# Kernel optimization log

Measured on AMD Instinct MI355X. Metric: run time of the kernel, lower is better.

The kernel has to match this reference:

```python
import jax, jax.numpy as jnp
import numpy as np

B, N, C_IN, C_OUT = 8, 4096, 512, 512


def setup_inputs() -> dict:
    key = jax.random.key(0)
    k1, k2, k3, k4 = jax.random.split(key, 4)
    node_features = jax.random.normal(k1, (B, N, C_IN), dtype=jnp.float32)
    # positive edge weights -> strictly positive degrees
    adj_matrix = jax.random.uniform(k2, (B, N, N), dtype=jnp.float32)
    W = jax.random.normal(k3, (C_IN, C_OUT), dtype=jnp.float32) / np.sqrt(C_IN)
    b = jax.random.normal(k4, (C_OUT,), dtype=jnp.float32) * 0.01
    return {"node_features": node_features, "adj_matrix": adj_matrix, "W": W, "b": b}


def reference(node_features, adj_matrix, W, b):
    # degree (row-sum of adjacency), kept as [B, N, 1] for broadcasting
    num_neighbours = adj_matrix.sum(axis=-1, keepdims=True)
    # linear projection: [B, N, c_in] @ [c_in, c_out] + b
    h = jnp.einsum("bni,io->bno", node_features, W) + b
    # adjacency aggregation: [B, N, N] @ [B, N, c_out]
    h = jnp.einsum("bnm,bmo->bno", adj_matrix, h)
    # mean over neighbours
    return h / num_neighbours
```

## Files before the change

### kernel.cpp

```cpp
#include <hip/hip_runtime.h>
#include <stdint.h>


typedef __attribute__((ext_vector_type(4))) float  f32x4;
typedef __attribute__((ext_vector_type(8))) __bf16 bf16x8;
typedef __attribute__((ext_vector_type(4))) __bf16 bf16x4;

#define GLOAD_LDS16(gsrc, ldst)                                                           \
  __builtin_amdgcn_global_load_lds((const __attribute__((address_space(1))) void*)(gsrc), \
                                   (__attribute__((address_space(3))) void*)(ldst), 16, 0, 0)

#define BARRIER                                  \
  do {                                           \
    asm volatile("" ::: "memory");               \
    __builtin_amdgcn_s_barrier();                \
    asm volatile("" ::: "memory");               \
  } while (0)

__global__ void __launch_bounds__(256) k_wt(const float* __restrict__ W,
                                            __bf16* __restrict__ Wt) {
  __shared__ __bf16 t[64][65];
  const int k0 = blockIdx.x * 64, n0 = blockIdx.y * 64;
  const int tid = threadIdx.x;
  const int r = tid >> 2, c4 = (tid & 3) * 16;
#pragma unroll
  for (int j = 0; j < 4; ++j) {
    f32x4 v = *reinterpret_cast<const f32x4*>(W + (size_t)(k0 + r) * 512 + n0 + c4 + j * 4);
#pragma unroll
    for (int q = 0; q < 4; ++q) t[c4 + j * 4 + q][r] = (__bf16)v[q];
  }
  __syncthreads();
#pragma unroll
  for (int j = 0; j < 4; ++j) {
    bf16x4 o;
#pragma unroll
    for (int q = 0; q < 4; ++q) o[q] = t[r][c4 + j * 4 + q];
    *reinterpret_cast<bf16x4*>(Wt + (size_t)(n0 + r) * 512 + k0 + c4 + j * 4) = o;
  }
}

__global__ void __launch_bounds__(256) k_proj(const float* __restrict__ X,
                                              const __bf16* __restrict__ Wt,
                                              const float* __restrict__ bias,
                                              __bf16* __restrict__ hT) {
  __shared__ __attribute__((aligned(16))) __bf16 Xs[128][72];
  __shared__ __attribute__((aligned(16))) __bf16 Ws[128][72];
  const int n0 = blockIdx.x * 128;
  const int m0 = blockIdx.y * 128;
  const int tid = threadIdx.x;
  const int lane = tid & 63, w = tid >> 6;
  const int wr = w >> 1, wc = w & 1;
  const int srow = tid >> 1, scb = (tid & 1) * 32;

  f32x4 acc[4][4] = {};

  for (int k0 = 0; k0 < 512; k0 += 64) {
    const float* xp = X + (size_t)(m0 + srow) * 512 + k0 + scb;
    f32x4 xv[8];
#pragma unroll
    for (int j = 0; j < 8; ++j) xv[j] = *reinterpret_cast<const f32x4*>(xp + j * 4);
#pragma unroll
    for (int q = 0; q < 4; ++q) {
      bf16x8 o;
#pragma unroll
      for (int e = 0; e < 8; ++e) { const int idx = q * 8 + e; o[e] = (__bf16)xv[idx >> 2][idx & 3]; }
      *reinterpret_cast<bf16x8*>(&Xs[srow][scb + q * 8]) = o;
    }
    const __bf16* wp = Wt + (size_t)(n0 + srow) * 512 + k0 + scb;
#pragma unroll
    for (int q = 0; q < 4; ++q)
      *reinterpret_cast<bf16x8*>(&Ws[srow][scb + q * 8]) =
          *reinterpret_cast<const bf16x8*>(wp + q * 8);
    __syncthreads();

    for (int kk = 0; kk < 64; kk += 32) {
      const int ko = kk + ((lane >> 4) << 3);
      bf16x8 a[4], bb[4];
#pragma unroll
      for (int i = 0; i < 4; ++i)
        a[i] = *reinterpret_cast<const bf16x8*>(&Xs[wr * 64 + i * 16 + (lane & 15)][ko]);
#pragma unroll
      for (int j = 0; j < 4; ++j)
        bb[j] = *reinterpret_cast<const bf16x8*>(&Ws[wc * 64 + j * 16 + (lane & 15)][ko]);
#pragma unroll
      for (int i = 0; i < 4; ++i)
#pragma unroll
        for (int j = 0; j < 4; ++j)
          acc[i][j] = __builtin_amdgcn_mfma_f32_16x16x32_bf16(a[i], bb[j], acc[i][j], 0, 0, 0);
    }
    __syncthreads();
  }

  float bj[4];
#pragma unroll
  for (int j = 0; j < 4; ++j) bj[j] = bias[n0 + wc * 64 + j * 16 + (lane & 15)];
  const int batch = m0 >> 12;
  const int mloc0 = (m0 & 4095) + wr * 64;
#pragma unroll
  for (int i = 0; i < 4; ++i) {
    const int m_in = mloc0 + i * 16 + ((lane >> 4) << 2);
#pragma unroll
    for (int j = 0; j < 4; ++j) {
      const int n = n0 + wc * 64 + j * 16 + (lane & 15);
      bf16x4 o;
#pragma unroll
      for (int r = 0; r < 4; ++r) o[r] = (__bf16)(acc[i][j][r] + bj[j]);
      *reinterpret_cast<bf16x4*>(hT + ((size_t)batch * 512 + n) * 4096 + m_in) = o;
    }
  }
}

__global__ void __launch_bounds__(1024, 4) k_agg(const float* __restrict__ adj,
                                                 const __bf16* __restrict__ hT,
                                                 float* __restrict__ out) {
  __shared__ __attribute__((aligned(16))) char lds[163840];
  char* As0 = lds;
  char* As1 = lds + 16384;
  char* Hs0 = lds + 32768;
  char* Hs1 = lds + 98304;

  const int bx = ((int)blockIdx.x & 7) * 32 + ((int)blockIdx.x >> 3);
  const int batch = bx >> 5;
  const int m0 = (bx & 31) * 128;
  const int tid = threadIdx.x;
  const int lane = tid & 63, w = tid >> 6;
  const int wr = w >> 3, wc = w & 7;

  const float*  adjb = adj + (size_t)batch * 4096 * 4096;
  const __bf16* hTb  = hT + (size_t)batch * 512 * 4096;
  float* outb = out + (size_t)batch * 4096 * 512;

  const int arow = tid >> 3;
  const int acb  = (tid & 7) * 8;
  const int aw   = arow * 128 + (((acb * 2)) ^ ((arow & 7) << 4));
  const float* adjrow = adjb + (size_t)(m0 + arow) * 4096 + acb;

  const int srcblk = (((lane & 7) ^ ((lane >> 3) & 7)) << 3);
  const int hrow_l = (lane >> 3);

  const int koffbase = (lane >> 4) << 3;
  const int kswz = (lane & 7) << 4;

  f32x4 acc[4][4] = {};
  float pdeg = 0.f;
  f32x4 av[2];

  auto load_adj = [&](int k0) {
    av[0] = __builtin_nontemporal_load(reinterpret_cast<const f32x4*>(adjrow + k0));
    av[1] = __builtin_nontemporal_load(reinterpret_cast<const f32x4*>(adjrow + k0 + 4));
  };
  auto issue_hs = [&](int k0, char* Hn) {
#pragma unroll
    for (int q = 0; q < 4; ++q) {
      const int c = w * 4 + q;
      const __bf16* src = hTb + (size_t)(c * 8 + hrow_l) * 4096 + k0 + srcblk;
      GLOAD_LDS16(src, Hn + c * 1024);
    }
  };
  auto write_as = [&](char* An) {
    bf16x8 o0;
#pragma unroll
    for (int e = 0; e < 8; ++e) o0[e] = (__bf16)av[e >> 2][e & 3];
    float s = 0.f;
#pragma unroll
    for (int e = 0; e < 8; ++e) s += av[e >> 2][e & 3];
    pdeg += s;
    *reinterpret_cast<bf16x8*>(An + aw) = o0;
  };
  auto compute = [&](const char* Ac, const char* Hc) {
#pragma unroll
    for (int kk = 0; kk < 64; kk += 32) {
      const int ko2 = ((kk + koffbase) * 2) ^ kswz;
      bf16x8 a[4], bb[4];
#pragma unroll
      for (int i = 0; i < 4; ++i) {
        const int row = wr * 64 + i * 16 + (lane & 15);
        a[i] = *reinterpret_cast<const bf16x8*>(Ac + row * 128 + ko2);
      }
#pragma unroll
      for (int j = 0; j < 4; ++j) {
        const int orow = wc * 64 + j * 16 + (lane & 15);
        bb[j] = *reinterpret_cast<const bf16x8*>(Hc + orow * 128 + ko2);
      }
#pragma unroll
      for (int i = 0; i < 4; ++i)
#pragma unroll
        for (int j = 0; j < 4; ++j)
          acc[i][j] = __builtin_amdgcn_mfma_f32_16x16x32_bf16(a[i], bb[j], acc[i][j], 0, 0, 0);
    }
  };

  load_adj(0);
  issue_hs(0, Hs0);
  write_as(As0);
  asm volatile("s_waitcnt vmcnt(0)" ::: "memory");
  asm volatile("s_waitcnt lgkmcnt(0)" ::: "memory");
  BARRIER;

  for (int t = 0; t < 63; ++t) {
    const int cur = t & 1;
    const char* Ac = cur ? As1 : As0;
    const char* Hc = cur ? Hs1 : Hs0;
    char* An = cur ? As0 : As1;
    char* Hn = cur ? Hs0 : Hs1;

    load_adj((t + 1) * 64);
    issue_hs((t + 1) * 64, Hn);
    compute(Ac, Hc);
    write_as(An);
    asm volatile("s_waitcnt vmcnt(0)" ::: "memory");
    asm volatile("s_waitcnt lgkmcnt(0)" ::: "memory");
    BARRIER;
  }

  compute(As1, Hs1);

  float d = pdeg;
  d += __shfl_xor(d, 1, 64);
  d += __shfl_xor(d, 2, 64);
  d += __shfl_xor(d, 4, 64);
  __syncthreads();
  if ((tid & 7) == 0) reinterpret_cast<float*>(lds)[arow] = d;
  __syncthreads();
  const float* degf = reinterpret_cast<const float*>(lds);

#pragma unroll
  for (int i = 0; i < 4; ++i) {
    const int rbase = wr * 64 + i * 16 + ((lane >> 4) << 2);
    float rd[4];
#pragma unroll
    for (int r = 0; r < 4; ++r) rd[r] = 1.0f / degf[rbase + r];
#pragma unroll
    for (int j = 0; j < 4; ++j) {
      const int o = wc * 64 + j * 16 + (lane & 15);
#pragma unroll
      for (int r = 0; r < 4; ++r)
        __builtin_nontemporal_store(acc[i][j][r] * rd[r],
                                    &outb[(size_t)(m0 + rbase + r) * 512 + o]);
    }
  }
}

extern "C" void kernel_launch(void* const* d_in, const int* in_sizes, int n_in,
                              void* d_out, int out_size, void* d_ws, size_t ws_size,
                              hipStream_t stream) {
  (void)in_sizes; (void)n_in; (void)out_size; (void)ws_size;
  const float* X    = (const float*)d_in[0];
  const float* adj  = (const float*)d_in[1];
  const float* W    = (const float*)d_in[2];
  const float* bias = (const float*)d_in[3];
  float* out = (float*)d_out;

  char* ws = (char*)d_ws;
  __bf16* hT = (__bf16*)ws;
  __bf16* Wt = (__bf16*)(ws + (size_t)32 * 1024 * 1024);

  k_wt<<<dim3(8, 8), 256, 0, stream>>>(W, Wt);
  k_proj<<<dim3(4, 256), 256, 0, stream>>>(X, Wt, bias, hT);
  k_agg<<<dim3(256), 1024, 0, stream>>>(adj, hT, out);
}
```

Measured before the change: 235.7 us.

## Prefetch adjacency tiles two iterations ahead with partial vmcnt waits

Adjacency loads now go into two alternating register sets and are issued two tiles ahead instead of one. The loop is unrolled by two to switch register sets, and it waits only on vmcnt(2), so the newest adjacency loads stay in flight across the barrier. This is meant to hide the global-memory latency of the large fp32 adjacency stream behind more MFMA work. It costs extra VGPRs and depends on the order in which memory counters complete, including the LDS-direct loads.

New measurement: 271.5 us. 15.2% more time.

```diff
diff --git a/kernel.cpp b/kernel.cpp
--- a/kernel.cpp
+++ b/kernel.cpp
@@ -143,12 +143,8 @@
 
   f32x4 acc[4][4] = {};
   float pdeg = 0.f;
-  f32x4 av[2];
-
-  auto load_adj = [&](int k0) {
-    av[0] = __builtin_nontemporal_load(reinterpret_cast<const f32x4*>(adjrow + k0));
-    av[1] = __builtin_nontemporal_load(reinterpret_cast<const f32x4*>(adjrow + k0 + 4));
-  };
+  f32x4 avA0, avA1, avB0, avB1;
+
   auto issue_hs = [&](int k0, char* Hn) {
 #pragma unroll
     for (int q = 0; q < 4; ++q) {
@@ -157,16 +153,6 @@
       GLOAD_LDS16(src, Hn + c * 1024);
     }
   };
-  auto write_as = [&](char* An) {
-    bf16x8 o0;
-#pragma unroll
-    for (int e = 0; e < 8; ++e) o0[e] = (__bf16)av[e >> 2][e & 3];
-    float s = 0.f;
-#pragma unroll
-    for (int e = 0; e < 8; ++e) s += av[e >> 2][e & 3];
-    pdeg += s;
-    *reinterpret_cast<bf16x8*>(An + aw) = o0;
-  };
   auto compute = [&](const char* Ac, const char* Hc) {
 #pragma unroll
     for (int kk = 0; kk < 64; kk += 32) {
@@ -190,30 +176,65 @@
     }
   };
 
-  load_adj(0);
+#define TILE_BODY(T, AVU0, AVU1, AVL0, AVL1, DOLOAD)                                      \
+  do {                                                                                    \
+    const int cur_ = (T) & 1;                                                             \
+    const char* Ac_ = cur_ ? As1 : As0;                                                   \
+    const char* Hc_ = cur_ ? Hs1 : Hs0;                                                   \
+    char* An_ = cur_ ? As0 : As1;                                                         \
+    char* Hn_ = cur_ ? Hs0 : Hs1;                                                         \
+    issue_hs(((T) + 1) * 64, Hn_);                                                        \
+    __builtin_amdgcn_sched_barrier(0);                \
+    if (DOLOAD) {                                                                         \
+      AVL0 = __builtin_nontemporal_load(                                                  \
+          reinterpret_cast<const f32x4*>(adjrow + ((T) + 2) * 64));                       \
+      AVL1 = __builtin_nontemporal_load(                                                  \
+          reinterpret_cast<const f32x4*>(adjrow + ((T) + 2) * 64 + 4));                   \
+    }                                                                                     \
+    compute(Ac_, Hc_);                                                                    \
+    {                                                                                     \
+      bf16x8 o0_;                                                                         \
+      _Pragma("unroll") for (int e = 0; e < 4; ++e) o0_[e] = (__bf16)AVU0[e];             \
+      _Pragma("unroll") for (int e = 0; e < 4; ++e) o0_[4 + e] = (__bf16)AVU1[e];         \
+      pdeg += AVU0[0] + AVU0[1] + AVU0[2] + AVU0[3] +                                     \
+              AVU1[0] + AVU1[1] + AVU1[2] + AVU1[3];                                      \
+      *reinterpret_cast<bf16x8*>(An_ + aw) = o0_;                                         \
+    }                                                                                     \
+    if (DOLOAD) { asm volatile("s_waitcnt vmcnt(2)" ::: "memory"); }                      \
+    else        { asm volatile("s_waitcnt vmcnt(0)" ::: "memory"); }                      \
+    asm volatile("s_waitcnt lgkmcnt(0)" ::: "memory");                                    \
+    BARRIER;                                                                              \
+  } while (0)
+
   issue_hs(0, Hs0);
-  write_as(As0);
-  asm volatile("s_waitcnt vmcnt(0)" ::: "memory");
+  __builtin_amdgcn_sched_barrier(0);
+  avA0 = __builtin_nontemporal_load(reinterpret_cast<const f32x4*>(adjrow));
+  avA1 = __builtin_nontemporal_load(reinterpret_cast<const f32x4*>(adjrow + 4));
+  {
+    bf16x8 o0;
+#pragma unroll
+    for (int e = 0; e < 4; ++e) o0[e] = (__bf16)avA0[e];
+#pragma unroll
+    for (int e = 0; e < 4; ++e) o0[4 + e] = (__bf16)avA1[e];
+    pdeg += avA0[0] + avA0[1] + avA0[2] + avA0[3] +
+            avA1[0] + avA1[1] + avA1[2] + avA1[3];
+    *reinterpret_cast<bf16x8*>(As0 + aw) = o0;
+  }
+  avA0 = __builtin_nontemporal_load(reinterpret_cast<const f32x4*>(adjrow + 64));
+  avA1 = __builtin_nontemporal_load(reinterpret_cast<const f32x4*>(adjrow + 68));
+  asm volatile("s_waitcnt vmcnt(2)" ::: "memory");
   asm volatile("s_waitcnt lgkmcnt(0)" ::: "memory");
   BARRIER;
 
-  for (int t = 0; t < 63; ++t) {
-    const int cur = t & 1;
-    const char* Ac = cur ? As1 : As0;
-    const char* Hc = cur ? Hs1 : Hs0;
-    char* An = cur ? As0 : As1;
-    char* Hn = cur ? Hs0 : Hs1;
-
-    load_adj((t + 1) * 64);
-    issue_hs((t + 1) * 64, Hn);
-    compute(Ac, Hc);
-    write_as(An);
-    asm volatile("s_waitcnt vmcnt(0)" ::: "memory");
-    asm volatile("s_waitcnt lgkmcnt(0)" ::: "memory");
-    BARRIER;
-  }
-
+  for (int tp = 0; tp < 31; ++tp) {
+    const int t0 = 2 * tp;
+    TILE_BODY(t0,     avA0, avA1, avB0, avB1, true);
+    TILE_BODY(t0 + 1, avB0, avB1, avA0, avA1, true);
+  }
+  TILE_BODY(62, avA0, avA1, avB0, avB1, false);
   compute(As1, Hs1);
+
+#undef TILE_BODY
 
   float d = pdeg;
   d += __shfl_xor(d, 1, 64);
```

## Load H operand directly from global into registers instead of staging in LDS

Applied to the files above, without the earlier changes.

The aggregation kernel no longer stages the transposed projection tile in double-buffered LDS via global_load_lds. Each wave now reads its B-fragments straight from global memory (expected to hit L2), which shrinks LDS from 160KB to about 33KB and removes the H-tile copy and its explicit waitcnt/barrier sequence. In exchange, every wave issues redundant global reads for the same H data with less latency hiding, since those loads sit directly in the MFMA loop.

Measured after the change: 394.8 us. 1.68x slower.

```diff
diff --git a/kernel.cpp b/kernel.cpp
--- a/kernel.cpp
+++ b/kernel.cpp
@@ -5,17 +5,6 @@
 typedef __attribute__((ext_vector_type(4))) float  f32x4;
 typedef __attribute__((ext_vector_type(8))) __bf16 bf16x8;
 typedef __attribute__((ext_vector_type(4))) __bf16 bf16x4;
-
-#define GLOAD_LDS16(gsrc, ldst)                                                           \
-  __builtin_amdgcn_global_load_lds((const __attribute__((address_space(1))) void*)(gsrc), \
-                                   (__attribute__((address_space(3))) void*)(ldst), 16, 0, 0)
-
-#define BARRIER                                  \
-  do {                                           \
-    asm volatile("" ::: "memory");               \
-    __builtin_amdgcn_s_barrier();                \
-    asm volatile("" ::: "memory");               \
-  } while (0)
 
 __global__ void __launch_bounds__(256) k_wt(const float* __restrict__ W,
                                             __bf16* __restrict__ Wt) {
@@ -113,11 +102,9 @@
 __global__ void __launch_bounds__(1024, 4) k_agg(const float* __restrict__ adj,
                                                  const __bf16* __restrict__ hT,
                                                  float* __restrict__ out) {
-  __shared__ __attribute__((aligned(16))) char lds[163840];
+  __shared__ __attribute__((aligned(16))) char lds[33280];
   char* As0 = lds;
   char* As1 = lds + 16384;
-  char* Hs0 = lds + 32768;
-  char* Hs1 = lds + 98304;
 
   const int bx = ((int)blockIdx.x & 7) * 32 + ((int)blockIdx.x >> 3);
   const int batch = bx >> 5;
@@ -132,42 +119,32 @@
 
   const int arow = tid >> 3;
   const int acb  = (tid & 7) * 8;
-  const int aw   = arow * 128 + (((acb * 2)) ^ ((arow & 7) << 4));
+  const int aw   = arow * 128 + ((acb * 2) ^ ((arow & 7) << 4));
   const float* adjrow = adjb + (size_t)(m0 + arow) * 4096 + acb;
-
-  const int srcblk = (((lane & 7) ^ ((lane >> 3) & 7)) << 3);
-  const int hrow_l = (lane >> 3);
 
   const int koffbase = (lane >> 4) << 3;
   const int kswz = (lane & 7) << 4;
 
+  const __bf16* hTw = hTb + (size_t)(wc * 64 + (lane & 15)) * 4096 + ((lane >> 4) << 3);
+
   f32x4 acc[4][4] = {};
   float pdeg = 0.f;
-  f32x4 av[2];
+  f32x4 av0, av1;
 
   auto load_adj = [&](int k0) {
-    av[0] = __builtin_nontemporal_load(reinterpret_cast<const f32x4*>(adjrow + k0));
-    av[1] = __builtin_nontemporal_load(reinterpret_cast<const f32x4*>(adjrow + k0 + 4));
-  };
-  auto issue_hs = [&](int k0, char* Hn) {
-#pragma unroll
-    for (int q = 0; q < 4; ++q) {
-      const int c = w * 4 + q;
-      const __bf16* src = hTb + (size_t)(c * 8 + hrow_l) * 4096 + k0 + srcblk;
-      GLOAD_LDS16(src, Hn + c * 1024);
-    }
+    av0 = __builtin_nontemporal_load(reinterpret_cast<const f32x4*>(adjrow + k0));
+    av1 = __builtin_nontemporal_load(reinterpret_cast<const f32x4*>(adjrow + k0 + 4));
   };
   auto write_as = [&](char* An) {
     bf16x8 o0;
 #pragma unroll
-    for (int e = 0; e < 8; ++e) o0[e] = (__bf16)av[e >> 2][e & 3];
-    float s = 0.f;
-#pragma unroll
-    for (int e = 0; e < 8; ++e) s += av[e >> 2][e & 3];
-    pdeg += s;
+    for (int e = 0; e < 4; ++e) o0[e] = (__bf16)av0[e];
+#pragma unroll
+    for (int e = 0; e < 4; ++e) o0[4 + e] = (__bf16)av1[e];
+    pdeg += av0[0] + av0[1] + av0[2] + av0[3] + av1[0] + av1[1] + av1[2] + av1[3];
     *reinterpret_cast<bf16x8*>(An + aw) = o0;
   };
-  auto compute = [&](const char* Ac, const char* Hc) {
+  auto compute = [&](const char* Ac, int kbase) {
 #pragma unroll
     for (int kk = 0; kk < 64; kk += 32) {
       const int ko2 = ((kk + koffbase) * 2) ^ kswz;
@@ -178,10 +155,8 @@
         a[i] = *reinterpret_cast<const bf16x8*>(Ac + row * 128 + ko2);
       }
 #pragma unroll
-      for (int j = 0; j < 4; ++j) {
-        const int orow = wc * 64 + j * 16 + (lane & 15);
-        bb[j] = *reinterpret_cast<const bf16x8*>(Hc + orow * 128 + ko2);
-      }
+      for (int j = 0; j < 4; ++j)
+        bb[j] = *reinterpret_cast<const bf16x8*>(hTw + (size_t)j * 16 * 4096 + kbase + kk);
 #pragma unroll
       for (int i = 0; i < 4; ++i)
 #pragma unroll
@@ -191,29 +166,20 @@
   };
 
   load_adj(0);
-  issue_hs(0, Hs0);
   write_as(As0);
-  asm volatile("s_waitcnt vmcnt(0)" ::: "memory");
-  asm volatile("s_waitcnt lgkmcnt(0)" ::: "memory");
-  BARRIER;
+  __syncthreads();
 
   for (int t = 0; t < 63; ++t) {
     const int cur = t & 1;
     const char* Ac = cur ? As1 : As0;
-    const char* Hc = cur ? Hs1 : Hs0;
     char* An = cur ? As0 : As1;
-    char* Hn = cur ? Hs0 : Hs1;
 
     load_adj((t + 1) * 64);
-    issue_hs((t + 1) * 64, Hn);
-    compute(Ac, Hc);
+    compute(Ac, t * 64);
     write_as(An);
-    asm volatile("s_waitcnt vmcnt(0)" ::: "memory");
-    asm volatile("s_waitcnt lgkmcnt(0)" ::: "memory");
-    BARRIER;
-  }
-
-  compute(As1, Hs1);
+    __syncthreads();
+  }
+  compute(As1, 63 * 64);
 
   float d = pdeg;
   d += __shfl_xor(d, 1, 64);
```
